# Performance work log

Measured on AMD Instinct MI355X. Metric: run time of the kernel, lower is better.

## Reference

```python
import jax, jax.numpy as jnp
import numpy as np

QMIN, QMAX = -128.0, 127.0


def _quant_dequant_act_8bit(x):
    # Dynamic per-row asymmetric 8-bit quantization of activations, then dequant.
    xmin = jnp.min(x, axis=-1, keepdims=True)
    xmax = jnp.max(x, axis=-1, keepdims=True)
    scale = jnp.maximum((xmax - xmin) / 255.0, 1e-8)
    zp = jnp.clip(jnp.round(QMIN - xmin / scale), QMIN, QMAX)
    qx = jnp.clip(jnp.round(x / scale) + zp, QMIN, QMAX)
    return (qx - zp) * scale


def setup_inputs() -> dict:
    key = jax.random.key(0)
    k_x, k_w, k_s, k_b = jax.random.split(key, 4)
    m, k, n, group_size = 32, 8192, 14336, 128
    n_groups = k // group_size  # 64
    x = jax.random.normal(k_x, (m, k), dtype=jnp.float32)
    # unsigned 4-bit codes in [0, 16); dequant uses (q - 8) * scale
    q_weight = jax.random.randint(k_w, (n, k), 0, 16, dtype=jnp.int32)
    w_scale = jax.random.uniform(k_s, (n, n_groups), dtype=jnp.float32) * 0.01 + 1e-3
    bias = jax.random.normal(k_b, (n,), dtype=jnp.float32) * 0.02
    return {"x": x, "q_weight": q_weight, "w_scale": w_scale, "bias": bias, "group_size": group_size}


def reference(x, q_weight, w_scale, bias, group_size):
    # _linear_8bit_act_4bit_weight: int8-act x 4-bit group-quantized weight GEMM + bias
    m, k = x.shape
    n = q_weight.shape[0]
    g = k // group_size
    x_dq = _quant_dequant_act_8bit(x).reshape(m, g, group_size)          # [m, g, gs]
    qw = (q_weight.astype(jnp.float32) - 8.0).reshape(n, g, group_size)  # [n, g, gs]
    # per-group partial products, then apply group scales and reduce over groups
    partial = jnp.einsum("mgc,ngc->mng", x_dq, qw)                        # [m, n, g]
    out = jnp.einsum("mng,ng->mn", partial, w_scale)                      # [m, n]
    return out + bias
```

## Files before the change

### kernel.cpp

```cpp
#include <hip/hip_runtime.h>
#include <hip/hip_bf16.h>

#define Mdim 32
#define Kdim 8192
#define Ndim 14336
#define GSZ  128
#define NGRP 64

#define KB 8
#define KC (Kdim/KB)
#define BN 128

typedef __attribute__((ext_vector_type(16))) float f32x16;
typedef __attribute__((ext_vector_type(8)))  short bf16x8;
typedef __attribute__((ext_vector_type(4)))  int   i32x4;

__global__ __launch_bounds__(256) void quant_rows_kernel(
        const float* __restrict__ x,
        __hip_bfloat16* __restrict__ xq,
        float* __restrict__ scales) {
    const int row = blockIdx.x;
    const float* xr = x + (size_t)row * Kdim;

    float lmin = 3.4e38f, lmax = -3.4e38f;
    for (int i = threadIdx.x; i < Kdim; i += 256) {
        const float v = xr[i];
        lmin = fminf(lmin, v);
        lmax = fmaxf(lmax, v);
    }
#pragma unroll
    for (int off = 32; off > 0; off >>= 1) {
        lmin = fminf(lmin, __shfl_xor(lmin, off, 64));
        lmax = fmaxf(lmax, __shfl_xor(lmax, off, 64));
    }
    __shared__ float smin[4], smax[4];
    const int wid = threadIdx.x >> 6;
    if ((threadIdx.x & 63) == 0) { smin[wid] = lmin; smax[wid] = lmax; }
    __syncthreads();
    const float xmin = fminf(fminf(smin[0], smin[1]), fminf(smin[2], smin[3]));
    const float xmax = fmaxf(fmaxf(smax[0], smax[1]), fmaxf(smax[2], smax[3]));

    const float scale = fmaxf((xmax - xmin) / 255.0f, 1e-8f);
    float zp = rintf(-128.0f - xmin / scale);
    zp = fminf(fmaxf(zp, -128.0f), 127.0f);
    if (threadIdx.x == 0) scales[row] = scale;

    for (int i = threadIdx.x; i < Kdim; i += 256) {
        float q = rintf(xr[i] / scale) + zp;
        q = fminf(fmaxf(q, -128.0f), 127.0f);
        xq[(size_t)row * Kdim + i] = __float2bfloat16(q - zp);
    }
}

__global__ __launch_bounds__(256) void init_out_kernel(
        const float* __restrict__ bias, float* __restrict__ out) {
    const int n = blockIdx.x * 256 + threadIdx.x;
    const int m = blockIdx.y;
    out[(size_t)m * Ndim + n] = bias[n];
}

__global__ __launch_bounds__(256) void qlin_main_kernel(
        const int* __restrict__ qw, const float* __restrict__ wscale,
        const __hip_bfloat16* __restrict__ xq, const float* __restrict__ scales,
        float* __restrict__ out) {
    const int lane  = threadIdx.x & 63;
    const int wid   = threadIdx.x >> 6;
    const int col   = blockIdx.x * BN + wid * 32 + (lane & 31);
    const int k0    = blockIdx.y * KC;
    const int khalf = (lane >> 5) * 8;

    const int* __restrict__ wp = qw + (size_t)col * Kdim + k0 + khalf;
    const __hip_bfloat16* __restrict__ ap =
        xq + (size_t)(lane & 31) * Kdim + k0 + khalf;
    const float* __restrict__ wsp = wscale + (size_t)col * NGRP + (k0 / GSZ);

    f32x16 acc = {};

    for (int g = 0; g < KC / GSZ; ++g) {
        const float ws   = wsp[g];
        const float m8ws = -8.0f * ws;
        const int* __restrict__ wpg = wp + g * GSZ;
        const __hip_bfloat16* __restrict__ apg = ap + g * GSZ;
#pragma unroll
        for (int s = 0; s < GSZ / 16; ++s) {
            const i32x4 q0 = __builtin_nontemporal_load((const i32x4*)(wpg + s * 16));
            const i32x4 q1 = __builtin_nontemporal_load((const i32x4*)(wpg + s * 16 + 4));
            const bf16x8 a = *(const bf16x8*)(apg + s * 16);

            union { bf16x8 v; __hip_bfloat162 h[4]; } bu;
            const float f0 = fmaf((float)q0[0], ws, m8ws);
            const float f1 = fmaf((float)q0[1], ws, m8ws);
            const float f2 = fmaf((float)q0[2], ws, m8ws);
            const float f3 = fmaf((float)q0[3], ws, m8ws);
            const float f4 = fmaf((float)q1[0], ws, m8ws);
            const float f5 = fmaf((float)q1[1], ws, m8ws);
            const float f6 = fmaf((float)q1[2], ws, m8ws);
            const float f7 = fmaf((float)q1[3], ws, m8ws);
            bu.h[0] = __float22bfloat162_rn(float2{f0, f1});
            bu.h[1] = __float22bfloat162_rn(float2{f2, f3});
            bu.h[2] = __float22bfloat162_rn(float2{f4, f5});
            bu.h[3] = __float22bfloat162_rn(float2{f6, f7});

            acc = __builtin_amdgcn_mfma_f32_32x32x16_bf16(a, bu.v, acc, 0, 0, 0);
        }
    }

    const int rbase = (lane >> 5) * 4;
#pragma unroll
    for (int r = 0; r < 16; ++r) {
        const int row = (r & 3) + 8 * (r >> 2) + rbase;
        unsafeAtomicAdd(out + (size_t)row * Ndim + col, scales[row] * acc[r]);
    }
}

extern "C" void kernel_launch(void* const* d_in, const int* in_sizes, int n_in,
                              void* d_out, int out_size, void* d_ws, size_t ws_size,
                              hipStream_t stream) {
    const float* x    = (const float*)d_in[0];
    const int*   qw   = (const int*)d_in[1];
    const float* wsc  = (const float*)d_in[2];
    const float* bias = (const float*)d_in[3];
    float* out = (float*)d_out;

    float* scales = (float*)d_ws;
    __hip_bfloat16* xq = (__hip_bfloat16*)((char*)d_ws + 256);

    quant_rows_kernel<<<Mdim, 256, 0, stream>>>(x, xq, scales);
    init_out_kernel<<<dim3(Ndim / 256, Mdim), 256, 0, stream>>>(bias, out);
    qlin_main_kernel<<<dim3(Ndim / BN, KB), 256, 0, stream>>>(qw, wsc, xq, scales, out);
}
```

Baseline: 754.2 us.

## Fuse bias init into quant kernel, shrink main block, vectorize loads

Folds the bias initialisation of the output into the activation quantization kernel, which removes one kernel launch. It also vectorizes the quant kernel's reads and writes with float4/ushort4 and preloads the per-row scales as float4 in the epilogue. The main GEMM now uses 64-column blocks of 128 threads, doubling the number of blocks, and the weight loads are changed from nontemporal to regular loads. Fusing bias init into a 32-block kernel may make that step slower, and dropping the nontemporal hint could change cache behaviour on the streaming weight reads.

```diff
diff --git a/kernel.cpp b/kernel.cpp
--- a/kernel.cpp
+++ b/kernel.cpp
@@ -9,7 +9,7 @@
 
 #define KB 8
 #define KC (Kdim/KB)
-#define BN 128
+#define BN 64
 
 typedef __attribute__((ext_vector_type(16))) float f32x16;
 typedef __attribute__((ext_vector_type(8)))  short bf16x8;
@@ -17,16 +17,19 @@
 
 __global__ __launch_bounds__(256) void quant_rows_kernel(
         const float* __restrict__ x,
+        const float* __restrict__ bias,
         __hip_bfloat16* __restrict__ xq,
-        float* __restrict__ scales) {
+        float* __restrict__ scales,
+        float* __restrict__ out) {
     const int row = blockIdx.x;
-    const float* xr = x + (size_t)row * Kdim;
+    const float4* __restrict__ xr4 = (const float4*)(x + (size_t)row * Kdim);
 
     float lmin = 3.4e38f, lmax = -3.4e38f;
-    for (int i = threadIdx.x; i < Kdim; i += 256) {
-        const float v = xr[i];
-        lmin = fminf(lmin, v);
-        lmax = fmaxf(lmax, v);
+#pragma unroll
+    for (int i = 0; i < Kdim / 4 / 256; ++i) {
+        const float4 v = xr4[threadIdx.x + i * 256];
+        lmin = fminf(lmin, fminf(fminf(v.x, v.y), fminf(v.z, v.w)));
+        lmax = fmaxf(lmax, fmaxf(fmaxf(v.x, v.y), fmaxf(v.z, v.w)));
     }
 #pragma unroll
     for (int off = 32; off > 0; off >>= 1) {
@@ -45,21 +48,31 @@
     zp = fminf(fmaxf(zp, -128.0f), 127.0f);
     if (threadIdx.x == 0) scales[row] = scale;
 
-    for (int i = threadIdx.x; i < Kdim; i += 256) {
-        float q = rintf(xr[i] / scale) + zp;
-        q = fminf(fmaxf(q, -128.0f), 127.0f);
-        xq[(size_t)row * Kdim + i] = __float2bfloat16(q - zp);
+    ushort4* __restrict__ xq4 = (ushort4*)(xq + (size_t)row * Kdim);
+#pragma unroll
+    for (int i = 0; i < Kdim / 4 / 256; ++i) {
+        const float4 v = xr4[threadIdx.x + i * 256];
+        ushort4 o;
+        float q;
+        q = fminf(fmaxf(rintf(v.x / scale) + zp, -128.0f), 127.0f);
+        o.x = __bfloat16_as_ushort(__float2bfloat16(q - zp));
+        q = fminf(fmaxf(rintf(v.y / scale) + zp, -128.0f), 127.0f);
+        o.y = __bfloat16_as_ushort(__float2bfloat16(q - zp));
+        q = fminf(fmaxf(rintf(v.z / scale) + zp, -128.0f), 127.0f);
+        o.z = __bfloat16_as_ushort(__float2bfloat16(q - zp));
+        q = fminf(fmaxf(rintf(v.w / scale) + zp, -128.0f), 127.0f);
+        o.w = __bfloat16_as_ushort(__float2bfloat16(q - zp));
+        xq4[threadIdx.x + i * 256] = o;
     }
+
+    const float4* __restrict__ b4 = (const float4*)bias;
+    float4* __restrict__ o4 = (float4*)(out + (size_t)row * Ndim);
+#pragma unroll
+    for (int i = 0; i < Ndim / 4 / 256; ++i)
+        o4[threadIdx.x + i * 256] = b4[threadIdx.x + i * 256];
 }
 
-__global__ __launch_bounds__(256) void init_out_kernel(
-        const float* __restrict__ bias, float* __restrict__ out) {
-    const int n = blockIdx.x * 256 + threadIdx.x;
-    const int m = blockIdx.y;
-    out[(size_t)m * Ndim + n] = bias[n];
-}
-
-__global__ __launch_bounds__(256) void qlin_main_kernel(
+__global__ __launch_bounds__(128) void qlin_main_kernel(
         const int* __restrict__ qw, const float* __restrict__ wscale,
         const __hip_bfloat16* __restrict__ xq, const float* __restrict__ scales,
         float* __restrict__ out) {
@@ -83,8 +96,8 @@
         const __hip_bfloat16* __restrict__ apg = ap + g * GSZ;
 #pragma unroll
         for (int s = 0; s < GSZ / 16; ++s) {
-            const i32x4 q0 = __builtin_nontemporal_load((const i32x4*)(wpg + s * 16));
-            const i32x4 q1 = __builtin_nontemporal_load((const i32x4*)(wpg + s * 16 + 4));
+            const i32x4 q0 = *(const i32x4*)(wpg + s * 16);
+            const i32x4 q1 = *(const i32x4*)(wpg + s * 16 + 4);
             const bf16x8 a = *(const bf16x8*)(apg + s * 16);
 
             union { bf16x8 v; __hip_bfloat162 h[4]; } bu;
@@ -106,10 +119,16 @@
     }
 
     const int rbase = (lane >> 5) * 4;
+    const float4 s0 = *(const float4*)(scales + rbase);
+    const float4 s1 = *(const float4*)(scales + rbase + 8);
+    const float4 s2 = *(const float4*)(scales + rbase + 16);
+    const float4 s3 = *(const float4*)(scales + rbase + 24);
+    const float sr[16] = {s0.x, s0.y, s0.z, s0.w, s1.x, s1.y, s1.z, s1.w,
+                          s2.x, s2.y, s2.z, s2.w, s3.x, s3.y, s3.z, s3.w};
 #pragma unroll
     for (int r = 0; r < 16; ++r) {
         const int row = (r & 3) + 8 * (r >> 2) + rbase;
-        unsafeAtomicAdd(out + (size_t)row * Ndim + col, scales[row] * acc[r]);
+        unsafeAtomicAdd(out + (size_t)row * Ndim + col, sr[r] * acc[r]);
     }
 }
 
@@ -125,7 +144,6 @@
     float* scales = (float*)d_ws;
     __hip_bfloat16* xq = (__hip_bfloat16*)((char*)d_ws + 256);
 
-    quant_rows_kernel<<<Mdim, 256, 0, stream>>>(x, xq, scales);
-    init_out_kernel<<<dim3(Ndim / 256, Mdim), 256, 0, stream>>>(bias, out);
-    qlin_main_kernel<<<dim3(Ndim / BN, KB), 256, 0, stream>>>(qw, wsc, xq, scales, out);
+    quant_rows_kernel<<<Mdim, 256, 0, stream>>>(x, bias, xq, scales, out);
+    qlin_main_kernel<<<dim3(Ndim / BN, KB), 128, 0, stream>>>(qw, wsc, xq, scales, out);
 }
```

New measurement: 635.0 us. 1.19x faster.
